# Kernel tuning notes

Measured on AMD Instinct MI355X. Metric: run time of the kernel, lower is better.

## Reference

```python
import jax, jax.numpy as jnp
import numpy as np

B, T, I, H, O = 64, 512, 512, 1024, 512


def setup_inputs() -> dict:
    key = jax.random.key(0)
    ks = jax.random.split(key, 11)
    s_gate = 1.0 / np.sqrt(I + H)
    s_fc = 1.0 / np.sqrt(H)
    return {
        "x": jax.random.normal(ks[0], (B, T, I), dtype=jnp.float32),
        "W_f": jax.random.uniform(ks[1], (H, I + H), jnp.float32, -s_gate, s_gate),
        "b_f": jax.random.uniform(ks[2], (H,), jnp.float32, -s_gate, s_gate),
        "W_i": jax.random.uniform(ks[3], (H, I + H), jnp.float32, -s_gate, s_gate),
        "b_i": jax.random.uniform(ks[4], (H,), jnp.float32, -s_gate, s_gate),
        "W_c": jax.random.uniform(ks[5], (H, I + H), jnp.float32, -s_gate, s_gate),
        "b_c": jax.random.uniform(ks[6], (H,), jnp.float32, -s_gate, s_gate),
        "W_o": jax.random.uniform(ks[7], (H, I + H), jnp.float32, -s_gate, s_gate),
        "b_o": jax.random.uniform(ks[8], (H,), jnp.float32, -s_gate, s_gate),
        "W_fc": jax.random.uniform(ks[9], (O, H), jnp.float32, -s_fc, s_fc),
        "b_fc": jax.random.uniform(ks[10], (O,), jnp.float32, -s_fc, s_fc),
    }


def reference(x, W_f, b_f, W_i, b_i, W_c, b_c, W_o, b_o, W_fc, b_fc):
    batch = x.shape[0]
    hidden = W_f.shape[0]
    # Concatenate the 4 gate weights into one GEMM per step (same math).
    W_all = jnp.concatenate([W_f, W_i, W_c, W_o], axis=0)   # [4H, I+H]
    b_all = jnp.concatenate([b_f, b_i, b_c, b_o], axis=0)   # [4H]

    def step(carry, x_t):
        h, c = carry
        combined = jnp.concatenate([x_t, h], axis=1)         # [B, I+H]
        gates = combined @ W_all.T + b_all                   # [B, 4H]
        f_t = jax.nn.sigmoid(gates[:, :hidden])
        i_t = jax.nn.sigmoid(gates[:, hidden:2 * hidden])
        c_tilde = jnp.tanh(gates[:, 2 * hidden:3 * hidden])
        o_t = jax.nn.sigmoid(gates[:, 3 * hidden:])
        c_new = f_t * c + i_t * c_tilde
        h_new = o_t * jnp.tanh(c_new)
        y = h_new @ W_fc.T + b_fc                            # [B, O]
        return (h_new, c_new), y

    h0 = jnp.zeros((batch, hidden), x.dtype)
    c0 = jnp.zeros((batch, hidden), x.dtype)
    (h, c), ys = jax.lax.scan(step, (h0, c0), jnp.swapaxes(x, 0, 1))
    return jnp.swapaxes(ys, 0, 1), (h, c)
```

## Files before the change

kernel.cpp:

```cpp
#include <hip/hip_runtime.h>
#include <stdint.h>

#define BB 64
#define TT 512
#define II 512
#define HH 1024
#define OO 512
#define NBLK 256
#define NTHR 512
#define NB 16
#define US 16

#define WS_HBUF  1280
#define WS_ASLAB 66816
#define WS_YSLAB 3212544
#define BTO (BB*TT*OO)
#define BH  (BB*HH)

#define L_HB_U4 1024
#define L_YP_F  12288
#define L_XP_F  (12288 + 1280)
#define L_BYTES ((13568 + 1024) * 4)

typedef __fp16 v8hf __attribute__((ext_vector_type(8)));
typedef float f32x4 __attribute__((ext_vector_type(4)));
typedef _Float16 h2 __attribute__((ext_vector_type(2)));

static __device__ __forceinline__ v8hf bc8(uint4 v) { return __builtin_bit_cast(v8hf, v); }
static __device__ __forceinline__ uint32_t pk_u32(float a, float b) {
  return __builtin_bit_cast(uint32_t, __builtin_amdgcn_cvt_pkrtz(a, b));
}

__device__ __forceinline__ float sigm(float v) { return 1.0f / (1.0f + __expf(-v)); }
__device__ __forceinline__ float tanh_c(float v) {
  v = fminf(fmaxf(v, -20.0f), 20.0f);
  float e = __expf(-2.0f * v);
  return (1.0f - e) / (1.0f + e);
}

__device__ __forceinline__ void burn64() {
  float a = 0.0f;
  #pragma unroll
  for (int i = 0; i < 64; ++i)
    asm volatile("v_fmac_f32 %0, %1, %1" : "+v"(a) : "v"(1.00001f));
  asm volatile("" :: "v"(a));
}

__device__ __forceinline__ uint2 cohere_ld8(const void* p) {
  unsigned long long q = __hip_atomic_load((const unsigned long long*)p,
                                           __ATOMIC_RELAXED, __HIP_MEMORY_SCOPE_AGENT);
  return __builtin_bit_cast(uint2, q);
}
__device__ __forceinline__ void cohere_st8(void* p, uint32_t lo, uint32_t hi) {
  uint2 v = make_uint2(lo, hi);
  __hip_atomic_store((unsigned long long*)p, __builtin_bit_cast(unsigned long long, v),
                     __ATOMIC_RELAXED, __HIP_MEMORY_SCOPE_AGENT);
}
__device__ __forceinline__ void cohere_st4(void* p, uint32_t v) {
  __hip_atomic_store((uint32_t*)p, v, __ATOMIC_RELAXED, __HIP_MEMORY_SCOPE_AGENT);
}

__global__ void __launch_bounds__(256) prep(
    const float* __restrict__ Wf, const float* __restrict__ Wi,
    const float* __restrict__ Wc, const float* __restrict__ Wo,
    const float* __restrict__ Wfc, float* __restrict__ ws)
{
  const int NA = 64 * 4 * 48 * 64;
  const int NY = 64 * 32 * 64;
  int idx = blockIdx.x * 256 + threadIdx.x;
  if (idx < NA) {
    int s = idx / (4 * 48 * 64);
    int rem = idx % (4 * 48 * 64);
    int mt = rem / (48 * 64);
    int rem2 = rem % (48 * 64);
    int ks = rem2 >> 6, ln = rem2 & 63;
    int r = ln & 15, kq = ln >> 4;
    int unit = s * 16 + mt * 4 + (r >> 2), gate = r & 3;
    const float* W = (gate == 0) ? Wf : (gate == 1) ? Wi : (gate == 2) ? Wc : Wo;
    const float* src = W + (size_t)unit * 1536 + ks * 32 + kq * 8;
    uint32_t p[4];
    #pragma unroll
    for (int j = 0; j < 4; ++j) {
      h2 t; t.x = (_Float16)src[2*j]; t.y = (_Float16)src[2*j+1];
      p[j] = __builtin_bit_cast(uint32_t, t);
    }
    ((uint4*)(ws + WS_ASLAB))[idx] = make_uint4(p[0], p[1], p[2], p[3]);
  } else if (idx < NA + NY) {
    int j2 = idx - NA;
    int s = j2 / (32 * 64);
    int rem = j2 % (32 * 64);
    int ks = rem >> 6, ln = rem & 63;
    int r = ln & 15, kq = ln >> 4;
    uint4 outv = make_uint4(0, 0, 0, 0);
    if (r < 8) {
      const float* src = Wfc + (size_t)(s * 8 + r) * 1024 + ks * 32 + kq * 8;
      uint32_t p[4];
      #pragma unroll
      for (int j = 0; j < 4; ++j) {
        h2 t; t.x = (_Float16)src[2*j]; t.y = (_Float16)src[2*j+1];
        p[j] = __builtin_bit_cast(uint32_t, t);
      }
      outv = make_uint4(p[0], p[1], p[2], p[3]);
    }
    ((uint4*)(ws + WS_YSLAB))[j2] = outv;
  }
}

__global__ void __launch_bounds__(NTHR, 2)
lstm_kernel(const float* __restrict__ x,
            const float* __restrict__ bf, const float* __restrict__ bi,
            const float* __restrict__ bc, const float* __restrict__ bo,
            const float* __restrict__ bfc,
            float* __restrict__ out, float* __restrict__ ws)
{
  extern __shared__ float ldsf[];
  uint4* acts4 = (uint4*)ldsf;
  float* ypart = ldsf + L_YP_F;
  float* xpart = ldsf + L_XP_F;

  const int tid  = threadIdx.x;
  const int blk  = blockIdx.x;
  const int wave = tid >> 6;
  const int lane = tid & 63;
  const bool isGate = (wave < 4);
  const int mt = wave & 3;
  const int g = blk >> 6, s = blk & 63;
  const int b0 = g * NB;
  const int u0 = s * US;

  uint32_t* ctrl  = (uint32_t*)ws;
  uint32_t* flags = ctrl + g * 128;
  ushort* hb16 = (ushort*)(ws + WS_HBUF);

  const int bq = lane & 15, kq = lane >> 4;
  const int tid2 = tid & 255;
  const int sb = tid2 >> 4, sj = tid2 & 15;
  const int gb = tid >> 5, gj = tid & 31;

  v8hf Ah[32];
  v8hf Ax[16];
  v8hf Yw[8];
  if (isGate) {
    const uint4* wpA = (const uint4*)(ws + WS_ASLAB)
                     + ((size_t)(s * 4 + mt) * 48 + 16) * 64 + lane;
    #pragma unroll
    for (int k = 0; k < 32; ++k) Ah[k] = bc8(wpA[k * 64]);
  } else {
    const uint4* wpA = (const uint4*)(ws + WS_ASLAB)
                     + ((size_t)(s * 4 + mt) * 48) * 64 + lane;
    #pragma unroll
    for (int k = 0; k < 16; ++k) Ax[k] = bc8(wpA[k * 64]);
    const uint4* wpY = (const uint4*)(ws + WS_YSLAB)
                     + ((size_t)(s * 32 + mt * 8)) * 64 + lane;
    #pragma unroll
    for (int k = 0; k < 8; ++k) Yw[k] = bc8(wpY[k * 64]);
  }
  const int unit = u0 + mt * 4 + kq;
  const float bsf = isGate ? bf[unit] : 0.f;
  const float bsi = isGate ? bi[unit] : 0.f;
  const float bsc = isGate ? bc[unit] : 0.f;
  const float bso = isGate ? bo[unit] : 0.f;
  const float ybias = (tid < 128) ? bfc[s * 8 + (tid >> 4)] : 0.0f;
  float cstate = 0.0f;

  if (!isGate) {
    const float* xs = x + ((size_t)(b0 + sb) * TT + 0) * II + sj * 32;
    #pragma unroll
    for (int v = 0; v < 4; ++v) {
      float4 u = ((const float4*)xs)[2*v], w = ((const float4*)xs)[2*v+1];
      acts4[sj * 64 + v * 16 + (sb ^ (sj & 7))] =
          make_uint4(pk_u32(u.x,u.y), pk_u32(u.z,u.w), pk_u32(w.x,w.y), pk_u32(w.z,w.w));
    }
  } else {
    #pragma unroll
    for (int j = 0; j < 8; ++j)
      acts4[L_HB_U4 + tid2 * 8 + j] = make_uint4(0,0,0,0);
  }
  __syncthreads();
  if (!isGate) {
    f32x4 ac[4];
    #pragma unroll
    for (int j = 0; j < 4; ++j) ac[j] = (f32x4){0.f,0.f,0.f,0.f};
    #pragma unroll
    for (int ks = 0; ks < 16; ++ks) {
      uint4 bv = acts4[ks * 64 + kq * 16 + (bq ^ (ks & 7))];
      ac[ks & 3] = __builtin_amdgcn_mfma_f32_16x16x32_f16(Ax[ks], bc8(bv), ac[ks & 3], 0, 0, 0);
    }
    f32x4 t = (ac[0] + ac[1]) + (ac[2] + ac[3]);
    float* xp = xpart + (mt * 64 + lane) * 4;
    xp[0] = t[0]; xp[1] = t[1]; xp[2] = t[2]; xp[3] = t[3];
  }
  __syncthreads();

  for (int it = 0; it <= TT; ++it) {
    const bool xok = (it + 1 < TT);

    if (isGate) {
      if (it < TT) {
        const float* xp = xpart + (mt * 64 + lane) * 4;
        f32x4 ac[4];
        ac[0] = (f32x4){xp[0], xp[1], xp[2], xp[3]};
        ac[1] = (f32x4){0.f,0.f,0.f,0.f};
        ac[2] = (f32x4){0.f,0.f,0.f,0.f};
        ac[3] = (f32x4){0.f,0.f,0.f,0.f};
        #pragma unroll
        for (int ksh = 0; ksh < 32; ++ksh) {
          uint4 bv = acts4[L_HB_U4 + ksh * 64 + kq * 16 + (bq ^ (ksh & 7))];
          ac[ksh & 3] = __builtin_amdgcn_mfma_f32_16x16x32_f16(Ah[ksh], bc8(bv), ac[ksh & 3], 0, 0, 0);
        }
        f32x4 t = (ac[0] + ac[1]) + (ac[2] + ac[3]);

        float gf = sigm(t[0] + bsf);
        float gi = sigm(t[1] + bsi);
        float gc = tanh_c(t[2] + bsc);
        float go = sigm(t[3] + bso);
        cstate = gf * cstate + gi * gc;
        float hv = go * tanh_c(cstate);

        uint32_t hu = (uint32_t)__builtin_bit_cast(unsigned short, (_Float16)hv);
        uint32_t pA  = hu | ((uint32_t)__shfl_down((int)hu, 16) << 16);
        uint32_t hiw = (uint32_t)__shfl_down((int)pA, 32);
        if (kq == 0) {
          ushort* hp = hb16 + (size_t)((it + 1) & 1) * BH
                     + (size_t)(b0 + bq) * HH + (u0 + mt * 4);
          cohere_st8(hp, pA, hiw);
        }
        if (it == TT - 1) {
          out[(size_t)BTO + (size_t)(b0 + bq) * HH + unit] = hv;
          out[(size_t)BTO + BH + (size_t)(b0 + bq) * HH + unit] = cstate;
        }
        asm volatile("s_waitcnt vmcnt(0)" ::: "memory");
      }
    } else {
      if (it > 0) {
        f32x4 yc = (f32x4){0.f,0.f,0.f,0.f};
        #pragma unroll
        for (int k = 0; k < 8; ++k) {
          int ksh = mt * 8 + k;
          uint4 bv = acts4[L_HB_U4 + ksh * 64 + kq * 16 + (bq ^ (ksh & 7))];
          yc = __builtin_amdgcn_mfma_f32_16x16x32_f16(Yw[k], bc8(bv), yc, 0, 0, 0);
        }
        float* yp = ypart + (mt * 64 + lane) * 5;
        yp[0] = yc[0]; yp[1] = yc[1]; yp[2] = yc[2]; yp[3] = yc[3];
      }
    }
    __syncthreads();

    if (it < TT && tid == 0)
      cohere_st4(&flags[s], (uint32_t)(it + 1));

    if (tid < 128 && it > 0) {
      int fb = tid & 15, rr = tid >> 4;
      int l = (rr >> 2) * 16 + fb;
      float yv = ybias;
      #pragma unroll
      for (int w = 0; w < 4; ++w) yv += ypart[(w * 64 + l) * 5 + (rr & 3)];
      out[(size_t)(b0 + fb) * (TT * OO) + (size_t)(it - 1) * OO + s * 8 + rr] = yv;
    }
    if (!isGate && xok) {
      const float* xs = x + ((size_t)(b0 + sb) * TT + (it + 1)) * II + sj * 32;
      float4 xr[8];
      #pragma unroll
      for (int v = 0; v < 8; ++v) xr[v] = ((const float4*)xs)[v];
      #pragma unroll
      for (int v = 0; v < 4; ++v)
        acts4[sj * 64 + v * 16 + (sb ^ (sj & 7))] =
            make_uint4(pk_u32(xr[2*v].x, xr[2*v].y), pk_u32(xr[2*v].z, xr[2*v].w),
                       pk_u32(xr[2*v+1].x, xr[2*v+1].y), pk_u32(xr[2*v+1].z, xr[2*v+1].w));
    }
    __syncthreads();

    if (!isGate && xok) {
      f32x4 ac[4];
      #pragma unroll
      for (int j = 0; j < 4; ++j) ac[j] = (f32x4){0.f,0.f,0.f,0.f};
      #pragma unroll
      for (int ks = 0; ks < 16; ++ks) {
        uint4 bv = acts4[ks * 64 + kq * 16 + (bq ^ (ks & 7))];
        ac[ks & 3] = __builtin_amdgcn_mfma_f32_16x16x32_f16(Ax[ks], bc8(bv), ac[ks & 3], 0, 0, 0);
      }
      f32x4 t = (ac[0] + ac[1]) + (ac[2] + ac[3]);
      float* xp = xpart + (mt * 64 + lane) * 4;
      xp[0] = t[0]; xp[1] = t[1]; xp[2] = t[2]; xp[3] = t[3];
    }

    if (it < TT) {
      {
        const uint32_t tgt = (uint32_t)(it + 1);
        for (;;) {
          uint2 f = cohere_ld8(&flags[gj * 2]);
          burn64();
          if (f.x >= tgt && f.y >= tgt) break;
        }
        const ushort* hs = hb16 + (size_t)((it + 1) & 1) * BH
                         + (size_t)(b0 + gb) * HH + gj * 32;
        uint2 q[8];
        #pragma unroll
        for (int m = 0; m < 8; ++m) q[m] = cohere_ld8(hs + m * 4);
        #pragma unroll
        for (int sub = 0; sub < 4; ++sub)
          acts4[L_HB_U4 + gj * 64 + sub * 16 + (gb ^ (gj & 7))] =
              make_uint4(q[2*sub].x, q[2*sub].y, q[2*sub+1].x, q[2*sub+1].y);
      }
      __syncthreads();
    }
  }
}

extern "C" void kernel_launch(void* const* d_in, const int* in_sizes, int n_in,
                              void* d_out, int out_size, void* d_ws, size_t ws_size,
                              hipStream_t stream) {
  (void)in_sizes; (void)n_in; (void)out_size; (void)ws_size;
  const float* x   = (const float*)d_in[0];
  const float* Wf  = (const float*)d_in[1];
  const float* bf  = (const float*)d_in[2];
  const float* Wi  = (const float*)d_in[3];
  const float* bi  = (const float*)d_in[4];
  const float* Wc  = (const float*)d_in[5];
  const float* bc  = (const float*)d_in[6];
  const float* Wo  = (const float*)d_in[7];
  const float* bo  = (const float*)d_in[8];
  const float* Wfc = (const float*)d_in[9];
  const float* bfc = (const float*)d_in[10];
  float* out = (float*)d_out;
  float* ws  = (float*)d_ws;

  (void)hipMemsetAsync(d_ws, 0, (size_t)WS_HBUF * sizeof(float), stream);

  const int nprep = 64 * 4 * 48 * 64 + 64 * 32 * 64;
  prep<<<dim3((nprep + 255) / 256), dim3(256), 0, stream>>>(Wf, Wi, Wc, Wo, Wfc, ws);

  lstm_kernel<<<dim3(NBLK), dim3(NTHR), L_BYTES, stream>>>(
      x, bf, bi, bc, bo, bfc, out, ws);
}
```

Measured before the change: 3.379 ms.

## Replace block barriers with LDS atomic barrier and per-wave global flags

Replaces the three per-step __syncthreads with a spin barrier built on an LDS atomic counter. Each gate wave now publishes its own progress flag right after storing its h slice, instead of one flag per block after a full block barrier. Consumers poll four times as many flags, and the spin burn is shortened from 64 to 16 FMAs. The aim is to cut latency on the cross-block recurrent handoff, at the cost of more polling traffic, busy-wait contention, and fragile memory-ordering assumptions.

```diff
diff --git a/kernel.cpp b/kernel.cpp
--- a/kernel.cpp
+++ b/kernel.cpp
@@ -20,7 +20,8 @@
 #define L_HB_U4 1024
 #define L_YP_F  12288
 #define L_XP_F  (12288 + 1280)
-#define L_BYTES ((13568 + 1024) * 4)
+#define L_BAR_F (L_XP_F + 1024)
+#define L_BYTES ((L_BAR_F + 16) * 4)
 
 typedef __fp16 v8hf __attribute__((ext_vector_type(8)));
 typedef float f32x4 __attribute__((ext_vector_type(4)));
@@ -38,12 +39,22 @@
   return (1.0f - e) / (1.0f + e);
 }
 
-__device__ __forceinline__ void burn64() {
+__device__ __forceinline__ void burn16() {
   float a = 0.0f;
   #pragma unroll
-  for (int i = 0; i < 64; ++i)
+  for (int i = 0; i < 16; ++i)
     asm volatile("v_fmac_f32 %0, %1, %1" : "+v"(a) : "v"(1.00001f));
   asm volatile("" :: "v"(a));
+}
+
+__device__ __forceinline__ void lds_barrier(uint32_t* bar, uint32_t ph, int lane) {
+  asm volatile("s_waitcnt lgkmcnt(0)" ::: "memory");
+  if (lane == 0)
+    (void)__hip_atomic_fetch_add(bar, 1u, __ATOMIC_RELAXED, __HIP_MEMORY_SCOPE_WORKGROUP);
+  while (__hip_atomic_load(bar, __ATOMIC_RELAXED, __HIP_MEMORY_SCOPE_WORKGROUP) < 8u * ph)
+    burn16();
+  __builtin_amdgcn_sched_barrier(0);
+  asm volatile("" ::: "memory");
 }
 
 __device__ __forceinline__ uint2 cohere_ld8(const void* p) {
@@ -117,6 +128,7 @@
   uint4* acts4 = (uint4*)ldsf;
   float* ypart = ldsf + L_YP_F;
   float* xpart = ldsf + L_XP_F;
+  uint32_t* bar = (uint32_t*)(ldsf + L_BAR_F);
 
   const int tid  = threadIdx.x;
   const int blk  = blockIdx.x;
@@ -129,7 +141,7 @@
   const int u0 = s * US;
 
   uint32_t* ctrl  = (uint32_t*)ws;
-  uint32_t* flags = ctrl + g * 128;
+  uint32_t* flags = ctrl + g * 256;
   ushort* hb16 = (ushort*)(ws + WS_HBUF);
 
   const int bq = lane & 15, kq = lane >> 4;
@@ -162,7 +174,9 @@
   const float bso = isGate ? bo[unit] : 0.f;
   const float ybias = (tid < 128) ? bfc[s * 8 + (tid >> 4)] : 0.0f;
   float cstate = 0.0f;
-
+  uint32_t bphase = 0;
+
+  if (tid == 0) *bar = 0;
   if (!isGate) {
     const float* xs = x + ((size_t)(b0 + sb) * TT + 0) * II + sj * 32;
     #pragma unroll
@@ -230,6 +244,7 @@
           out[(size_t)BTO + BH + (size_t)(b0 + bq) * HH + unit] = cstate;
         }
         asm volatile("s_waitcnt vmcnt(0)" ::: "memory");
+        if (lane == 0) cohere_st4(&flags[s * 4 + mt], (uint32_t)(it + 1));
       }
     } else {
       if (it > 0) {
@@ -244,10 +259,7 @@
         yp[0] = yc[0]; yp[1] = yc[1]; yp[2] = yc[2]; yp[3] = yc[3];
       }
     }
-    __syncthreads();
-
-    if (it < TT && tid == 0)
-      cohere_st4(&flags[s], (uint32_t)(it + 1));
+    lds_barrier(bar, ++bphase, lane);
 
     if (tid < 128 && it > 0) {
       int fb = tid & 15, rr = tid >> 4;
@@ -268,7 +280,7 @@
             make_uint4(pk_u32(xr[2*v].x, xr[2*v].y), pk_u32(xr[2*v].z, xr[2*v].w),
                        pk_u32(xr[2*v+1].x, xr[2*v+1].y), pk_u32(xr[2*v+1].z, xr[2*v+1].w));
     }
-    __syncthreads();
+    lds_barrier(bar, ++bphase, lane);
 
     if (!isGate && xok) {
       f32x4 ac[4];
@@ -287,10 +299,15 @@
     if (it < TT) {
       {
         const uint32_t tgt = (uint32_t)(it + 1);
+        const uint32_t* fp = &flags[gj * 8];
         for (;;) {
-          uint2 f = cohere_ld8(&flags[gj * 2]);
-          burn64();
-          if (f.x >= tgt && f.y >= tgt) break;
+          uint2 f0 = cohere_ld8(fp + 0);
+          uint2 f1 = cohere_ld8(fp + 2);
+          uint2 f2 = cohere_ld8(fp + 4);
+          uint2 f3 = cohere_ld8(fp + 6);
+          burn16();
+          if (f0.x >= tgt && f0.y >= tgt && f1.x >= tgt && f1.y >= tgt &&
+              f2.x >= tgt && f2.y >= tgt && f3.x >= tgt && f3.y >= tgt) break;
         }
         const ushort* hs = hb16 + (size_t)((it + 1) & 1) * BH
                          + (size_t)(b0 + gb) * HH + gj * 32;
@@ -302,7 +319,7 @@
           acts4[L_HB_U4 + gj * 64 + sub * 16 + (gb ^ (gj & 7))] =
               make_uint4(q[2*sub].x, q[2*sub].y, q[2*sub+1].x, q[2*sub+1].y);
       }
-      __syncthreads();
+      lds_barrier(bar, ++bphase, lane);
     }
   }
 }
```

Result: slower. 3.512 ms (+3.9%).
